# Kernel tuning notes

Measured on AMD Instinct MI355X. Metric: run time of the kernel, lower is better.

Reference implementation:

```python
import jax, jax.numpy as jnp
import numpy as np

NUM_JOINTS = 17

def _build_norm_adj():
    # Same skeleton as _get_skeleton_edges, made bidirectional; row-normalized
    # so that A @ x computes the per-node mean over neighbors (every joint
    # has degree >= 1, matching the original's mean aggregation branch).
    conns = [(0, 7), (7, 8), (8, 9), (9, 10), (0, 1), (1, 2), (2, 3), (0, 4),
             (4, 5), (5, 6), (8, 11), (11, 12), (12, 13), (8, 14), (14, 15), (15, 16)]
    A = np.zeros((NUM_JOINTS, NUM_JOINTS), dtype=np.float32)
    for a, b in conns:
        A[a, b] = 1.0
        A[b, a] = 1.0
    deg = A.sum(axis=1, keepdims=True)
    A = A / np.maximum(deg, 1.0)
    return jnp.asarray(A)

def _xavier(key, out_dim, in_dim):
    lim = np.sqrt(6.0 / (in_dim + out_dim)).astype(np.float32)
    return jax.random.uniform(key, (out_dim, in_dim), jnp.float32, -lim, lim)

def setup_inputs() -> dict:
    key = jax.random.key(0)
    ks = jax.random.split(key, 6)
    B, J, D_IN, H, D_OUT = 65536, NUM_JOINTS, 3, 64, 256
    x = jax.random.normal(ks[0], (B, J, D_IN), jnp.float32)
    return {
        "x": x,
        "A": _build_norm_adj(),
        "W1": _xavier(ks[1], H, D_IN), "b1": jnp.zeros((H,), jnp.float32),
        "W2": _xavier(ks[2], H, H),    "b2": jnp.zeros((H,), jnp.float32),
        "W3": _xavier(ks[3], H, H),    "b3": jnp.zeros((H,), jnp.float32),
        "Wp1": _xavier(ks[4], H, J * H), "bp1": jnp.zeros((H,), jnp.float32),
        "Wp2": _xavier(ks[5], D_OUT, H), "bp2": jnp.zeros((D_OUT,), jnp.float32),
    }

def reference(x, A, W1, b1, W2, b2, W3, b3, Wp1, bp1, Wp2, bp2):
    # GCN layer 1: neighbor-mean aggregate then linear (+ReLU; dropout = eval identity)
    h = jnp.einsum('ij,bjd->bid', A, x)            # (B, 17, 3)
    h = jax.nn.relu(h @ W1.T + b1)                 # (B, 17, 64)
    # GCN layer 2
    h = jnp.einsum('ij,bjd->bid', A, h)
    h = jax.nn.relu(h @ W2.T + b2)
    # GCN layer 3 (no activation)
    h = jnp.einsum('ij,bjd->bid', A, h)
    h = h @ W3.T + b3                              # (B, 17, 64)
    # Global pool MLP over flattened joints
    flat = h.reshape(h.shape[0], -1)               # (B, 17*64)
    z = jax.nn.relu(flat @ Wp1.T + bp1)            # (B, 64)
    return z @ Wp2.T + bp2                         # (B, 256)
```

## Files before the change

kernel.cpp:

```cpp
#include <hip/hip_runtime.h>
#include <hip/hip_bf16.h>
#include <stdint.h>

typedef __attribute__((ext_vector_type(8))) short short8;
typedef __attribute__((ext_vector_type(4))) float f32x4;
typedef __attribute__((ext_vector_type(4))) unsigned int u32x4;
typedef __attribute__((ext_vector_type(2))) unsigned int u32x2;

constexpr int kNBR[17][4] = {
    {7, 1, 4, 0}, {0, 2, 0, 0}, {1, 3, 0, 0}, {2, 0, 0, 0},
    {0, 5, 0, 0}, {4, 6, 0, 0}, {5, 0, 0, 0}, {0, 8, 0, 0},
    {7, 9, 11, 14}, {8, 10, 0, 0}, {9, 0, 0, 0}, {8, 12, 0, 0},
    {11, 13, 0, 0}, {12, 0, 0, 0}, {8, 15, 0, 0}, {14, 16, 0, 0},
    {15, 0, 0, 0}};
constexpr int kDEG[17] = {3,2,2,1,2,2,1,2,4,2,1,2,2,1,2,2,1};
constexpr float kRDEG[5] = {0.f, 1.f, 0.5f, 0.33333334f, 0.25f};
constexpr int kWNT[4] = {3, 4, 5, 5};
constexpr int kWJT[4][5] = {{8, 1, 2, 0, 0},
                            {0, 4, 5, 3, 0},
                            {7, 9, 11, 6, 10},
                            {12, 14, 15, 13, 16}};
constexpr uint32_t kNBO(int i) {
  return (uint32_t)(kNBR[i][0] * 3) | ((uint32_t)(kNBR[i][1] * 3) << 8) |
         ((uint32_t)(kNBR[i][2] * 3) << 16) | ((uint32_t)(kNBR[i][3] * 3) << 24);
}

__device__ inline unsigned short f2bf(float f) {
  union { float f; uint32_t u; } v; v.f = f;
  uint32_t u = v.u;
  uint32_t r = u + 0x7fffu + ((u >> 16) & 1u);
  return (unsigned short)(r >> 16);
}
__device__ inline uint32_t pk2(float a, float b) {
  union { __hip_bfloat162 h; uint32_t u; } v;
  v.h = __float22bfloat162_rn(make_float2(a, b));
  return v.u;
}
__device__ inline f32x4 mfma16(short8 a, short8 b, f32x4 c) {
  return __builtin_amdgcn_mfma_f32_16x16x32_bf16(a, b, c, 0, 0, 0);
}

__global__ void prep(const float* __restrict__ W1,
                     const float* __restrict__ W2,
                     const float* __restrict__ Wp2,
                     const float* __restrict__ W3,
                     const float* __restrict__ Wp1,
                     const float* __restrict__ b3,
                     const float* __restrict__ bp1,
                     const float* __restrict__ b1,
                     short* __restrict__ W1b,
                     short* __restrict__ W2b,
                     short* __restrict__ Wp2b,
                     short* __restrict__ Mb,
                     float* __restrict__ bp1p) {
  __shared__ float w3s[4096];
  __shared__ float Qs[256];
  const int tid = threadIdx.x;
  const int bx = blockIdx.x;
  if (bx < 272) {
    for (int q = tid; q < 4096; q += 256) w3s[q] = W3[q];
    {
      int ro = tid >> 6, k = tid & 63;
      int r = bx * 4 + ro;
      int f = r / 17, i = r - f * 17;
      int dj = kDEG[i];
      float s = 0.f;
#pragma unroll
      for (int t = 0; t < 4; t++) {
        if (t < dj) {
          int nb = kNBR[i][t];
          s += kRDEG[kDEG[nb]] * Wp1[f * 1088 + nb * 64 + k];
        }
      }
      Qs[ro * 64 + k] = s;
    }
    __syncthreads();
    {
      int ro = tid >> 6, c = tid & 63;
      int r = bx * 4 + ro;
      int f = r / 17, i = r - f * 17;
      float s = 0.f;
#pragma unroll
      for (int k = 0; k < 64; k++) s += Qs[ro * 64 + k] * w3s[k * 64 + c];
      int h = c >> 5;
      int c5 = c & 31;
      int q = (c5 >> 2) & 3;
      int m = ((c5 >> 4) << 2) | (c5 & 3);
      int w = f >> 4, l15 = f & 15;
      Mb[((((w * 17 + i) * 2 + h) * 64) + q * 16 + l15) * 8 + m] = (short)f2bf(s);
    }
  } else if (bx < 360) {
    int q = (bx - 272) * 256 + tid;
    if (q < 4096) {
      int r = q >> 6, c = q & 63;
      int h = c >> 5, c5 = c & 31;
      int qq = (c5 >> 2) & 3, m = ((c5 >> 4) << 2) | (c5 & 3);
      W2b[r * 64 + h * 32 + qq * 8 + m] = (short)f2bf(W2[q]);
    }
    int q2 = q - 4096;
    if (q2 >= 0 && q2 < 16384) {
      int r = q2 >> 6, c = q2 & 63;
      int h = c >> 5, c5 = c & 31;
      int qq = (c5 >> 2) & 3, m = ((c5 >> 4) << 2) | (c5 & 3);
      Wp2b[r * 64 + h * 32 + qq * 8 + m] = (short)f2bf(Wp2[q2]);
    }
    int q3 = q - 20480;
    if (q3 >= 0 && q3 < 2048) {
      int row = q3 >> 5, k = q3 & 31;
      int c = k & 7;
      short v = 0;
      if (c < 3) v = (short)f2bf(W1[row * 3 + c]);
      else if (k == 3) v = (short)f2bf(b1[row]);
      W1b[q3] = v;
    }
  } else {
    int wv = tid >> 6, l = tid & 63;
    int f = (bx - 360) * 4 + wv;
    float s = 0.f;
#pragma unroll
    for (int i = 0; i < 17; i++) s += Wp1[f * 1088 + i * 64 + l] * b3[l];
#pragma unroll
    for (int off = 32; off > 0; off >>= 1) s += __shfl_down(s, off);
    if (l == 0) bp1p[f] = bp1[f] + s;
  }
}

template <int WV>
__device__ __forceinline__ void waveBody(
    const short* __restrict__ Mb2, const short* __restrict__ Wp2p,
    const short* __restrict__ W2p, const float* __restrict__ bp2g,
    float* __restrict__ OUT, float* __restrict__ pbuf,
    float* __restrict__ xs, float* __restrict__ sbias,
    const short8 (&w1f)[4], int bx, int lane, int ln15, int quad) {
  constexpr int NT = kWNT[WV];
  const int xbase = ln15 * 51;
  const int q8 = quad * 8;
  const float bias1 = (quad == 0) ? 1.0f : 0.0f;

  short8 w2f[2][4];
#pragma unroll
  for (int h = 0; h < 2; h++)
#pragma unroll
    for (int ft = 0; ft < 4; ft++)
      w2f[h][ft] = *(const short8*)(W2p + (ft * 16 + ln15) * 64 + h * 32 + quad * 8);

  u32x4 pkh2q[2][NT][2];
#pragma unroll
  for (int t = 0; t < NT; t++) {
    const int j = kWJT[WV][t];
    const int dj = kDEG[j];
    const float wj = kRDEG[dj];
    u32x4 ph1q[4][2][2];
#pragma unroll
    for (int s = 0; s < 4; s++) {
      if (s < dj) {
        const int i = kNBR[j][s];
        const int di = kDEG[i];
        const float wi = kRDEG[di];
        const int off = (int)((kNBO(i) >> q8) & 0xffu);
        const int b = xbase + off;
        const float wq = (quad < di) ? wi : 0.f;
#pragma unroll
        for (int g = 0; g < 2; g++) {
          const float* xsg = xs + g * 816;
          union { short8 s8; u32x4 u; } fr;
          fr.u.x = pk2(xsg[b] * wq, xsg[b + 1] * wq);
          fr.u.y = pk2(xsg[b + 2] * wq, bias1);
          fr.u.z = 0u;
          fr.u.w = 0u;
          f32x4 a[4];
#pragma unroll
          for (int ft = 0; ft < 4; ft++)
            a[ft] = mfma16(w1f[ft], fr.s8, (f32x4){0.f, 0.f, 0.f, 0.f});
          u32x4 q0, q1;
          q0.x = pk2(fmaxf(a[0].x, 0.f), fmaxf(a[0].y, 0.f));
          q0.y = pk2(fmaxf(a[0].z, 0.f), fmaxf(a[0].w, 0.f));
          q0.z = pk2(fmaxf(a[1].x, 0.f), fmaxf(a[1].y, 0.f));
          q0.w = pk2(fmaxf(a[1].z, 0.f), fmaxf(a[1].w, 0.f));
          q1.x = pk2(fmaxf(a[2].x, 0.f), fmaxf(a[2].y, 0.f));
          q1.y = pk2(fmaxf(a[2].z, 0.f), fmaxf(a[2].w, 0.f));
          q1.z = pk2(fmaxf(a[3].x, 0.f), fmaxf(a[3].y, 0.f));
          q1.w = pk2(fmaxf(a[3].z, 0.f), fmaxf(a[3].w, 0.f));
          ph1q[s][g][0] = q0;
          ph1q[s][g][1] = q1;
        }
      }
    }
#pragma unroll
    for (int g = 0; g < 2; g++) {
      f32x4 a[4];
#pragma unroll
      for (int ft = 0; ft < 4; ft++) a[ft] = (f32x4){0.f, 0.f, 0.f, 0.f};
#pragma unroll
      for (int s = 0; s < 4; s++)
        if (s < dj) {
#pragma unroll
          for (int h = 0; h < 2; h++) {
            union { u32x4 u; short8 s8; } bf;
            bf.u = ph1q[s][g][h];
#pragma unroll
            for (int ft = 0; ft < 4; ft++)
              a[ft] = mfma16(w2f[h][ft], bf.s8, a[ft]);
          }
        }
      u32x4 qq[2];
#pragma unroll
      for (int ft = 0; ft < 4; ft++) {
        int fb = ft * 16 + quad * 4;
        f32x4 bv = *(const f32x4*)&sbias[fb];
        uint32_t lo = pk2(fmaxf(a[ft].x * wj + bv.x, 0.f),
                          fmaxf(a[ft].y * wj + bv.y, 0.f));
        uint32_t hi = pk2(fmaxf(a[ft].z * wj + bv.z, 0.f),
                          fmaxf(a[ft].w * wj + bv.w, 0.f));
        if (ft & 1) { qq[ft >> 1].z = lo; qq[ft >> 1].w = hi; }
        else        { qq[ft >> 1].x = lo; qq[ft >> 1].y = hi; }
      }
      pkh2q[g][t][0] = qq[0];
      pkh2q[g][t][1] = qq[1];
    }
  }

  f32x4 zacc[4][2];
#pragma unroll
  for (int w4 = 0; w4 < 4; w4++) {
    zacc[w4][0] = (f32x4){0.f, 0.f, 0.f, 0.f};
    zacc[w4][1] = (f32x4){0.f, 0.f, 0.f, 0.f};
  }
  const short8* mb = (const short8*)Mb2;
#pragma unroll
  for (int t = 0; t < NT; t++) {
    const int i = kWJT[WV][t];
#pragma unroll
    for (int h = 0; h < 2; h++) {
      union { u32x4 u; short8 s8; } bf0, bf1;
      bf0.u = pkh2q[0][t][h];
      bf1.u = pkh2q[1][t][h];
#pragma unroll
      for (int w4 = 0; w4 < 4; w4++) {
        short8 af = mb[(((w4 * 17 + i) * 2 + h) * 64) + lane];
        zacc[w4][0] = mfma16(af, bf0.s8, zacc[w4][0]);
        zacc[w4][1] = mfma16(af, bf1.s8, zacc[w4][1]);
      }
    }
  }
#pragma unroll
  for (int w4 = 0; w4 < 4; w4++)
#pragma unroll
    for (int g = 0; g < 2; g++)
      *(f32x4*)(pbuf + WV * 2048 + (w4 * 2 + g) * 256 + lane * 4) = zacc[w4][g];
  short8 wp2f[4][2];
#pragma unroll
  for (int t = 0; t < 4; t++) {
    int ot = WV + 4 * t;
    wp2f[t][0] = *(const short8*)(Wp2p + (ot * 16 + ln15) * 64 + quad * 8);
    wp2f[t][1] = *(const short8*)(Wp2p + (ot * 16 + ln15) * 64 + 32 + quad * 8);
  }
  __syncthreads();

  u32x4 zpq[2][2];
#pragma unroll
  for (int w4 = 0; w4 < 4; w4++) {
    f32x4 bv = *(const f32x4*)&sbias[64 + w4 * 16 + quad * 4];
#pragma unroll
    for (int g = 0; g < 2; g++) {
      const int gw = w4 * 2 + g;
      f32x4 s0 = *(const f32x4*)(pbuf + 0 * 2048 + gw * 256 + lane * 4);
      f32x4 s1 = *(const f32x4*)(pbuf + 1 * 2048 + gw * 256 + lane * 4);
      f32x4 s2 = *(const f32x4*)(pbuf + 2 * 2048 + gw * 256 + lane * 4);
      f32x4 s3 = *(const f32x4*)(pbuf + 3 * 2048 + gw * 256 + lane * 4);
      f32x4 s = (s0 + s1) + (s2 + s3);
      uint32_t lo = pk2(fmaxf(s.x + bv.x, 0.f), fmaxf(s.y + bv.y, 0.f));
      uint32_t hi = pk2(fmaxf(s.z + bv.z, 0.f), fmaxf(s.w + bv.w, 0.f));
      if (w4 & 1) { zpq[g][w4 >> 1].z = lo; zpq[g][w4 >> 1].w = hi; }
      else        { zpq[g][w4 >> 1].x = lo; zpq[g][w4 >> 1].y = hi; }
    }
  }

  const int e0 = bx * 32;
#pragma unroll
  for (int g = 0; g < 2; g++) {
    union { u32x4 u; short8 s8; } bf0, bf1;
    bf0.u = zpq[g][0];
    bf1.u = zpq[g][1];
    int e0g = e0 + g * 16;
#pragma unroll
    for (int t = 0; t < 4; t++) {
      int ot = WV + 4 * t;
      f32x4 a = mfma16(wp2f[t][0], bf0.s8, (f32x4){0.f, 0.f, 0.f, 0.f});
      a = mfma16(wp2f[t][1], bf1.s8, a);
      int ob = ot * 16 + quad * 4;
      f32x4 bv = *(const f32x4*)&bp2g[ob];
      f32x4 res = a + bv;
      *(f32x4*)(OUT + (size_t)(e0g + ln15) * 256 + ob) = res;
    }
  }
}

__launch_bounds__(256, 2)
__global__ void gcn_main(const float* __restrict__ X,
                         const short* __restrict__ Mb2,
                         const short* __restrict__ Wp2p,
                         const short* __restrict__ W2p,
                         const short* __restrict__ W1b,
                         const float* __restrict__ bp1p,
                         const float* __restrict__ b2g,
                         const float* __restrict__ bp2g,
                         float* __restrict__ OUT) {
  __shared__ __align__(16) float pbuf[8192];
  __shared__ __align__(16) float xs[2 * 816];
  __shared__ __align__(16) float sbias[128];

  const int tid = threadIdx.x;
  const int wave = tid >> 6;
  const int lane = tid & 63;
  const int ln15 = lane & 15;
  const int quad = lane >> 4;
  const int bx = blockIdx.x;

  for (int q = tid; q < 408; q += 256)
    ((f32x4*)xs)[q] = ((const f32x4*)(X + (size_t)bx * 1632))[q];
  short8 w1f[4];
#pragma unroll
  for (int ft = 0; ft < 4; ft++)
    w1f[ft] = *(const short8*)(W1b + (ft * 16 + (lane & 15)) * 32 + (lane >> 4) * 8);
  if (tid < 128) sbias[tid] = (tid < 64) ? b2g[tid] : bp1p[tid - 64];
  __syncthreads();

  if (wave == 0)
    waveBody<0>(Mb2, Wp2p, W2p, bp2g, OUT, pbuf, xs, sbias, w1f, bx, lane, ln15, quad);
  else if (wave == 1)
    waveBody<1>(Mb2, Wp2p, W2p, bp2g, OUT, pbuf, xs, sbias, w1f, bx, lane, ln15, quad);
  else if (wave == 2)
    waveBody<2>(Mb2, Wp2p, W2p, bp2g, OUT, pbuf, xs, sbias, w1f, bx, lane, ln15, quad);
  else
    waveBody<3>(Mb2, Wp2p, W2p, bp2g, OUT, pbuf, xs, sbias, w1f, bx, lane, ln15, quad);
}

extern "C" void kernel_launch(void* const* d_in, const int* in_sizes, int n_in,
                              void* d_out, int out_size, void* d_ws, size_t ws_size,
                              hipStream_t stream) {
  const float* X = (const float*)d_in[0];
  const float* W1 = (const float*)d_in[2];
  const float* b1 = (const float*)d_in[3];
  const float* W2 = (const float*)d_in[4];
  const float* b2 = (const float*)d_in[5];
  const float* W3 = (const float*)d_in[6];
  const float* b3 = (const float*)d_in[7];
  const float* Wp1 = (const float*)d_in[8];
  const float* bp1 = (const float*)d_in[9];
  const float* Wp2 = (const float*)d_in[10];
  const float* bp2 = (const float*)d_in[11];
  float* OUT = (float*)d_out;
  const int B = in_sizes[0] / 51;

  char* ws = (char*)d_ws;
  short* Mb = (short*)(ws + 0);
  short* Wp2b = (short*)(ws + 139264);
  short* W2b = (short*)(ws + 172032);
  short* W1b = (short*)(ws + 180224);
  float* bp1p = (float*)(ws + 184320);

  prep<<<376, 256, 0, stream>>>(W1, W2, Wp2, W3, Wp1, b3, bp1, b1,
                                W1b, W2b, Wp2b, Mb, bp1p);
  gcn_main<<<B / 32, 256, 0, stream>>>(X, Mb, Wp2b, W2b, W1b, bp1p,
                                       b2, bp2, OUT);
}
```

Baseline: 143.4 us.

## Interleave per-joint GCN stages into streaming accumulation and raise occupancy

Restructures the per-wave body so each joint's layer-1 output is consumed immediately by the layer-2 MFMAs, and each joint's layer-2 result goes straight into the pooled projection accumulators. This removes the large live arrays ph1q and pkh2q that held all neighbors and joints in registers. The launch bound is raised from 2 to 3 blocks per SM to use the freed registers for occupancy. The risk is less independent MFMA work available for scheduling, and possible spills if the compiler cannot fit the tighter register budget.

```diff
diff --git a/kernel.cpp b/kernel.cpp
--- a/kernel.cpp
+++ b/kernel.cpp
@@ -144,13 +144,25 @@
     for (int ft = 0; ft < 4; ft++)
       w2f[h][ft] = *(const short8*)(W2p + (ft * 16 + ln15) * 64 + h * 32 + quad * 8);
 
-  u32x4 pkh2q[2][NT][2];
+  const short8* mb = (const short8*)Mb2;
+  f32x4 zacc[4][2];
+#pragma unroll
+  for (int w4 = 0; w4 < 4; w4++) {
+    zacc[w4][0] = (f32x4){0.f, 0.f, 0.f, 0.f};
+    zacc[w4][1] = (f32x4){0.f, 0.f, 0.f, 0.f};
+  }
+
 #pragma unroll
   for (int t = 0; t < NT; t++) {
     const int j = kWJT[WV][t];
     const int dj = kDEG[j];
     const float wj = kRDEG[dj];
-    u32x4 ph1q[4][2][2];
+    f32x4 a2[2][4];
+#pragma unroll
+    for (int g = 0; g < 2; g++)
+#pragma unroll
+      for (int ft = 0; ft < 4; ft++) a2[g][ft] = (f32x4){0.f, 0.f, 0.f, 0.f};
+
 #pragma unroll
     for (int s = 0; s < 4; s++) {
       if (s < dj) {
@@ -160,6 +172,7 @@
         const int off = (int)((kNBO(i) >> q8) & 0xffu);
         const int b = xbase + off;
         const float wq = (quad < di) ? wi : 0.f;
+        u32x4 pht[2][2];
 #pragma unroll
         for (int g = 0; g < 2; g++) {
           const float* xsg = xs + g * 816;
@@ -181,68 +194,51 @@
           q1.y = pk2(fmaxf(a[2].z, 0.f), fmaxf(a[2].w, 0.f));
           q1.z = pk2(fmaxf(a[3].x, 0.f), fmaxf(a[3].y, 0.f));
           q1.w = pk2(fmaxf(a[3].z, 0.f), fmaxf(a[3].w, 0.f));
-          ph1q[s][g][0] = q0;
-          ph1q[s][g][1] = q1;
+          pht[g][0] = q0;
+          pht[g][1] = q1;
         }
-      }
-    }
-#pragma unroll
-    for (int g = 0; g < 2; g++) {
-      f32x4 a[4];
-#pragma unroll
-      for (int ft = 0; ft < 4; ft++) a[ft] = (f32x4){0.f, 0.f, 0.f, 0.f};
-#pragma unroll
-      for (int s = 0; s < 4; s++)
-        if (s < dj) {
+#pragma unroll
+        for (int g = 0; g < 2; g++)
 #pragma unroll
           for (int h = 0; h < 2; h++) {
             union { u32x4 u; short8 s8; } bf;
-            bf.u = ph1q[s][g][h];
+            bf.u = pht[g][h];
 #pragma unroll
             for (int ft = 0; ft < 4; ft++)
-              a[ft] = mfma16(w2f[h][ft], bf.s8, a[ft]);
+              a2[g][ft] = mfma16(w2f[h][ft], bf.s8, a2[g][ft]);
           }
-        }
-      u32x4 qq[2];
+      }
+    }
+
+    u32x4 pkt[2][2];
+#pragma unroll
+    for (int g = 0; g < 2; g++) {
 #pragma unroll
       for (int ft = 0; ft < 4; ft++) {
         int fb = ft * 16 + quad * 4;
         f32x4 bv = *(const f32x4*)&sbias[fb];
-        uint32_t lo = pk2(fmaxf(a[ft].x * wj + bv.x, 0.f),
-                          fmaxf(a[ft].y * wj + bv.y, 0.f));
-        uint32_t hi = pk2(fmaxf(a[ft].z * wj + bv.z, 0.f),
-                          fmaxf(a[ft].w * wj + bv.w, 0.f));
-        if (ft & 1) { qq[ft >> 1].z = lo; qq[ft >> 1].w = hi; }
-        else        { qq[ft >> 1].x = lo; qq[ft >> 1].y = hi; }
+        uint32_t lo = pk2(fmaxf(a2[g][ft].x * wj + bv.x, 0.f),
+                          fmaxf(a2[g][ft].y * wj + bv.y, 0.f));
+        uint32_t hi = pk2(fmaxf(a2[g][ft].z * wj + bv.z, 0.f),
+                          fmaxf(a2[g][ft].w * wj + bv.w, 0.f));
+        if (ft & 1) { pkt[g][ft >> 1].z = lo; pkt[g][ft >> 1].w = hi; }
+        else        { pkt[g][ft >> 1].x = lo; pkt[g][ft >> 1].y = hi; }
       }
-      pkh2q[g][t][0] = qq[0];
-      pkh2q[g][t][1] = qq[1];
-    }
-  }
-
-  f32x4 zacc[4][2];
-#pragma unroll
-  for (int w4 = 0; w4 < 4; w4++) {
-    zacc[w4][0] = (f32x4){0.f, 0.f, 0.f, 0.f};
-    zacc[w4][1] = (f32x4){0.f, 0.f, 0.f, 0.f};
-  }
-  const short8* mb = (const short8*)Mb2;
-#pragma unroll
-  for (int t = 0; t < NT; t++) {
-    const int i = kWJT[WV][t];
+    }
 #pragma unroll
     for (int h = 0; h < 2; h++) {
       union { u32x4 u; short8 s8; } bf0, bf1;
-      bf0.u = pkh2q[0][t][h];
-      bf1.u = pkh2q[1][t][h];
+      bf0.u = pkt[0][h];
+      bf1.u = pkt[1][h];
 #pragma unroll
       for (int w4 = 0; w4 < 4; w4++) {
-        short8 af = mb[(((w4 * 17 + i) * 2 + h) * 64) + lane];
+        short8 af = mb[(((w4 * 17 + j) * 2 + h) * 64) + lane];
         zacc[w4][0] = mfma16(af, bf0.s8, zacc[w4][0]);
         zacc[w4][1] = mfma16(af, bf1.s8, zacc[w4][1]);
       }
     }
   }
+
 #pragma unroll
   for (int w4 = 0; w4 < 4; w4++)
 #pragma unroll
@@ -296,7 +292,7 @@
   }
 }
 
-__launch_bounds__(256, 2)
+__launch_bounds__(256, 3)
 __global__ void gcn_main(const float* __restrict__ X,
                          const short* __restrict__ Mb2,
                          const short* __restrict__ Wp2p,
```

After: 199.0 us. 1.39x slower.
